# Kernel optimization log

Hardware: AMD Instinct MI355X
Metric: run time of the kernel (lower is better)

The kernel has to match this reference:

```python
import jax, jax.numpy as jnp
import numpy as np
from jax import lax

F_CNT = 64    # factories per player
U_CNT = 2048  # units per player
GRID = 16     # spatial map side after stride-3 conv on 48x48 board


def conv2d(x, w, b, stride=1, pad=1):
    return lax.conv_general_dilated(x, w, (stride, stride), [(pad, pad), (pad, pad)],
                                    dimension_numbers=('NCHW', 'OIHW', 'NCHW')) + b[None, :, None, None]


def prelu(x, a):
    return jnp.where(x > 0, x, a * x)


def linear(x, w, b):
    return x @ w.T + b


def layernorm(x, g, b, eps=1e-5):
    mu = jnp.mean(x, -1, keepdims=True)
    var = jnp.mean((x - mu) ** 2, -1, keepdims=True)
    return (x - mu) / jnp.sqrt(var + eps) * g + b


def maxpool2(x):
    return lax.reduce_window(x, -jnp.inf, lax.max, (1, 1, 2, 2), (1, 1, 2, 2), 'VALID')


def mha4(f0, u0, f1, u1, fw, fb, uw, ub, lw, lb, num_heads=2, hidden=32):
    # FourSequenceMHAttention: per head, per player, separate Q/K/V linears for
    # factories and units; sequence order is [fac_p0, units_p0, fac_p1, units_p1].
    scale = hidden ** 0.5
    heads = []
    for h in range(num_heads):
        Q, K, V = [], [], []
        for i, (f, u) in enumerate(((f0, u0), (f1, u1))):
            b0 = h * 6 + i * 3
            Q.append(linear(f, fw[b0], fb[b0]))
            K.append(linear(f, fw[b0 + 1], fb[b0 + 1]))
            V.append(linear(f, fw[b0 + 2], fb[b0 + 2]))
            Q.append(linear(u, uw[b0], ub[b0]))
            K.append(linear(u, uw[b0 + 1], ub[b0 + 1]))
            V.append(linear(u, uw[b0 + 2], ub[b0 + 2]))
        Qc = jnp.concatenate(Q, 1)
        Kc = jnp.concatenate(K, 1)
        Vc = jnp.concatenate(V, 1)
        attn = jax.nn.softmax(jnp.einsum('bqd,bkd->bqk', Qc, Kc) / scale, axis=-1)
        heads.append(jnp.einsum('bqk,bkd->bqd', attn, Vc))
    return linear(jnp.concatenate(heads, -1), lw, lb)


def scatter_mask(feat, pos, C):
    # one-hot scatter-add of per-unit features onto the 16x16 grid (batch==1)
    gm = jnp.zeros((GRID, GRID, C), feat.dtype).at[pos[:, 0], pos[:, 1]].add(feat[0])
    return jnp.transpose(gm, (2, 0, 1))[None]  # [1,C,16,16]


def _forward(fl, p0_fac_pos, p0_unit_pos, p1_fac_pos, p1_unit_pos):
    (board, p0_fac_feat, p0_unit_feat, p1_fac_feat, p1_unit_feat,
     sp_w1, sp_b1, sp_a1, sp_w2, sp_b2, sp_a2, sp_w3, sp_b3,
     enc_fac_w, enc_fac_b, enc_unit_w, enc_unit_b, enc_lin_w, enc_lin_b,
     ext_fac_w, ext_fac_b, ext_unit_w, ext_unit_b, ext_lin_w, ext_lin_b, ext_ln_g, ext_ln_b,
     v_w1, v_b1, v_a1, v_w2, v_b2, v_a2, v_lw, v_lb,
     fo_w1, fo_b1, fo_a, fo_w2, fo_b2, ro_w1, ro_b1, ro_a, ro_w2, ro_b2) = fl

    sm = prelu(conv2d(board, sp_w1, sp_b1), sp_a1)
    sm = prelu(conv2d(sm, sp_w2, sp_b2), sp_a2)
    sm = conv2d(sm, sp_w3, sp_b3, stride=3, pad=0)  # [1,24,16,16]

    def gather(pos):
        # per-unit gather of the 24-dim spatial feature at (pos_x, pos_y)
        return jnp.transpose(sm[0][:, pos[:, 0], pos[:, 1]], (1, 0))[None]  # [1,N,24]

    f0 = jnp.concatenate([p0_fac_feat, gather(p0_fac_pos)], -1)    # [1,F,31]
    u0 = jnp.concatenate([p0_unit_feat, gather(p0_unit_pos)], -1)  # [1,U,38]
    f1 = jnp.concatenate([p1_fac_feat, gather(p1_fac_pos)], -1)
    u1 = jnp.concatenate([p1_unit_feat, gather(p1_unit_pos)], -1)

    gmu0 = scatter_mask(p0_unit_feat, p0_unit_pos, 14)
    gmf0 = scatter_mask(p0_fac_feat, p0_fac_pos, 7)
    gmu1 = scatter_mask(p1_unit_feat, p1_unit_pos, 14)
    gmf1 = scatter_mask(p1_fac_feat, p1_fac_pos, 7)
    # loop prepends each team's masks: after p1 order is [u1, f1, u0, f0, spatial]
    v_map = jnp.concatenate([gmu1, gmf1, gmu0, gmf0, sm], 1)  # [1,66,16,16]

    seq = mha4(f0, u0, f1, u1, enc_fac_w, enc_fac_b, enc_unit_w, enc_unit_b, enc_lin_w, enc_lin_b)
    S0, S1, S2 = F_CNT, F_CNT + U_CNT, 2 * F_CNT + U_CNT
    for l in range(2):
        new = mha4(seq[:, :S0], seq[:, S0:S1], seq[:, S1:S2], seq[:, S2:],
                   ext_fac_w[l], ext_fac_b[l], ext_unit_w[l], ext_unit_b[l],
                   ext_lin_w[l], ext_lin_b[l])
        seq = layernorm(seq + new, ext_ln_g[l], ext_ln_b[l])

    def head2(x, w1, b1, a, w2, b2):
        return linear(prelu(linear(x, w1, b1), a), w2, b2)

    f0o = head2(seq[:, :S0], fo_w1, fo_b1, fo_a, fo_w2, fo_b2)      # [1,F,4]
    u0o = head2(seq[:, S0:S1], ro_w1, ro_b1, ro_a, ro_w2, ro_b2)    # [1,U,17]
    f1o = head2(seq[:, S1:S2], fo_w1, fo_b1, fo_a, fo_w2, fo_b2)
    u1o = head2(seq[:, S2:], ro_w1, ro_b1, ro_a, ro_w2, ro_b2)

    vm = maxpool2(prelu(conv2d(v_map, v_w1, v_b1), v_a1))  # [1,96,8,8]
    vm = maxpool2(prelu(conv2d(vm, v_w2, v_b2), v_a2))     # [1,128,4,4]
    v = jnp.tanh(vm.reshape(vm.shape[0], -1) @ v_lw.T + v_lb)  # [1,1]
    return (f0o, u0o, f1o, u1o, v)


def setup_inputs() -> dict:
    key = jax.random.key(0)
    ks = iter(jax.random.split(key, 64))

    def rn(shape, s=1.0):
        return s * jax.random.normal(next(ks), shape, dtype=jnp.float32)

    def ri(shape):
        return jax.random.randint(next(ks), shape, 0, GRID)

    a25 = lambda: jnp.full((1,), 0.25, jnp.float32)  # torch PReLU default
    inp = {
        'board': rn((1, 14, 48, 48)),
        'p0_fac_feat': rn((1, F_CNT, 7)), 'p0_unit_feat': rn((1, U_CNT, 14)),
        'p1_fac_feat': rn((1, F_CNT, 7)), 'p1_unit_feat': rn((1, U_CNT, 14)),
        'sp_w1': rn((48, 14, 3, 3), 0.05), 'sp_b1': rn((48,), 0.05), 'sp_a1': a25(),
        'sp_w2': rn((96, 48, 3, 3), 0.05), 'sp_b2': rn((96,), 0.05), 'sp_a2': a25(),
        'sp_w3': rn((24, 96, 3, 3), 0.05), 'sp_b3': rn((24,), 0.05),
        'enc_fac_w': rn((12, 32, 31), 0.05), 'enc_fac_b': rn((12, 32), 0.05),
        'enc_unit_w': rn((12, 32, 38), 0.05), 'enc_unit_b': rn((12, 32), 0.05),
        'enc_lin_w': rn((32, 64), 0.05), 'enc_lin_b': rn((32,), 0.05),
        'ext_fac_w': rn((2, 12, 32, 32), 0.05), 'ext_fac_b': rn((2, 12, 32), 0.05),
        'ext_unit_w': rn((2, 12, 32, 32), 0.05), 'ext_unit_b': rn((2, 12, 32), 0.05),
        'ext_lin_w': rn((2, 32, 64), 0.05), 'ext_lin_b': rn((2, 32), 0.05),
        'ext_ln_g': jnp.ones((2, 32), jnp.float32), 'ext_ln_b': jnp.zeros((2, 32), jnp.float32),
        'v_w1': rn((96, 66, 3, 3), 0.05), 'v_b1': rn((96,), 0.05), 'v_a1': a25(),
        'v_w2': rn((128, 96, 3, 3), 0.05), 'v_b2': rn((128,), 0.05), 'v_a2': a25(),
        'v_lw': rn((1, 128 * 16), 0.05), 'v_lb': rn((1,), 0.05),
        'fo_w1': rn((32, 32), 0.05), 'fo_b1': rn((32,), 0.05), 'fo_a': a25(),
        'fo_w2': rn((4, 32), 0.05), 'fo_b2': rn((4,), 0.05),
        'ro_w1': rn((32, 32), 0.05), 'ro_b1': rn((32,), 0.05), 'ro_a': a25(),
        'ro_w2': rn((17, 32), 0.05), 'ro_b2': rn((17,), 0.05),
        'p0_fac_pos': ri((F_CNT, 2)), 'p0_unit_pos': ri((U_CNT, 2)),
        'p1_fac_pos': ri((F_CNT, 2)), 'p1_unit_pos': ri((U_CNT, 2)),
    }
    return inp


def reference(board, p0_fac_feat, p0_unit_feat, p1_fac_feat, p1_unit_feat,
              sp_w1, sp_b1, sp_a1, sp_w2, sp_b2, sp_a2, sp_w3, sp_b3,
              enc_fac_w, enc_fac_b, enc_unit_w, enc_unit_b, enc_lin_w, enc_lin_b,
              ext_fac_w, ext_fac_b, ext_unit_w, ext_unit_b, ext_lin_w, ext_lin_b, ext_ln_g, ext_ln_b,
              v_w1, v_b1, v_a1, v_w2, v_b2, v_a2, v_lw, v_lb,
              fo_w1, fo_b1, fo_a, fo_w2, fo_b2, ro_w1, ro_b1, ro_a, ro_w2, ro_b2,
              p0_fac_pos, p0_unit_pos, p1_fac_pos, p1_unit_pos):
    fl = (board, p0_fac_feat, p0_unit_feat, p1_fac_feat, p1_unit_feat,
          sp_w1, sp_b1, sp_a1, sp_w2, sp_b2, sp_a2, sp_w3, sp_b3,
          enc_fac_w, enc_fac_b, enc_unit_w, enc_unit_b, enc_lin_w, enc_lin_b,
          ext_fac_w, ext_fac_b, ext_unit_w, ext_unit_b, ext_lin_w, ext_lin_b, ext_ln_g, ext_ln_b,
          v_w1, v_b1, v_a1, v_w2, v_b2, v_a2, v_lw, v_lb,
          fo_w1, fo_b1, fo_a, fo_w2, fo_b2, ro_w1, ro_b1, ro_a, ro_w2, ro_b2)
    return _forward(fl, p0_fac_pos, p0_unit_pos, p1_fac_pos, p1_unit_pos)
```

## Files before the change

### kernel.cpp

```cpp
#include <hip/hip_runtime.h>
#include <hip/hip_bf16.h>

#define SEQ 4224
#define KSPLIT 11
#define KITERS 6
typedef unsigned int uint;
typedef unsigned short ushort;
typedef __attribute__((ext_vector_type(8))) short bf16x8;
typedef __attribute__((ext_vector_type(4))) float f32x4;

__device__ __forceinline__ float prelu_f(float x, float a){ return x > 0.f ? x : a*x; }

__device__ __forceinline__ ushort bfr(float x){
  uint u = __float_as_uint(x);
  u = (u + 0x7fffu + ((u>>16)&1u)) >> 16;
  return (ushort)u;
}
__device__ __forceinline__ uint pkbf(float a, float b){
  __hip_bfloat162 h2 = __float22bfloat162_rn(make_float2(a,b));
  union { __hip_bfloat162 h; uint u; } cv; cv.h = h2; return cv.u;
}

#define QSCALE 0.25505607190037247f
#define FIXEDM 8.0f

struct MegaParams {
  const float *board,*p0f,*p0u,*p1f,*p1u;
  const float *sp_w1,*sp_b1,*sp_a1,*sp_w2,*sp_b2,*sp_a2,*sp_w3,*sp_b3;
  const float *enc_fac_w,*enc_fac_b,*enc_unit_w,*enc_unit_b,*enc_lin_w,*enc_lin_b;
  const float *ext_fac_w,*ext_fac_b,*ext_unit_w,*ext_unit_b,*ext_lin_w,*ext_lin_b,*ext_ln_g,*ext_ln_b;
  const float *v_w1,*v_b1,*v_a1,*v_w2,*v_b2,*v_a2,*v_lw,*v_lb;
  const float *fo_w1,*fo_b1,*fo_a,*fo_w2,*fo_b2,*ro_w1,*ro_b1,*ro_a,*ro_w2,*ro_b2;
  const int *p0fp,*p0up,*p1fp,*p1up;
  float* out;
  float *sm1,*sm2,*sm;
  ushort *q16,*k16,*vt16;
  float *Hp,*auxl,*seqA,*seqB,*vmap,*vp1,*vp2;
};

template<int CIN, int HW, int CPT>
__device__ __forceinline__ void conv_item(int cg_, int pxb, int tid,
    const float* __restrict__ in, const float* __restrict__ w,
    const float* __restrict__ bias, const float* __restrict__ alpha,
    float* __restrict__ out, float* SF){
  float* Ws = SF;
  float* Bs = SF + CPT*CIN*9;
  for (int idx=tid; idx<CPT*CIN*9; idx+=256) Ws[idx] = w[cg_*CPT*CIN*9 + idx];
  if (tid<CPT) Bs[tid] = bias[cg_*CPT+tid];
  __syncthreads();
  int p = pxb*256 + tid;
  int x = p % HW, y = p / HW;
  float a = alpha[0];
  float acc[CPT];
  #pragma unroll
  for (int c=0;c<CPT;++c) acc[c]=Bs[c];
  #pragma unroll 2
  for (int i=0;i<CIN;++i){
    const float* ip = in + i*HW*HW;
    float win[9];
    #pragma unroll
    for (int ky=0;ky<3;++ky){
      int yy = y+ky-1;
      #pragma unroll
      for (int kx=0;kx<3;++kx){
        int xx = x+kx-1;
        bool ok = ((unsigned)yy < (unsigned)HW) && ((unsigned)xx < (unsigned)HW);
        win[ky*3+kx] = ok ? ip[yy*HW+xx] : 0.f;
      }
    }
    #pragma unroll
    for (int c=0;c<CPT;++c){
      const float* wp = &Ws[(c*CIN+i)*9];
      #pragma unroll
      for (int k=0;k<9;++k) acc[c] += win[k]*wp[k];
    }
  }
  #pragma unroll
  for (int c=0;c<CPT;++c)
    out[(cg_*CPT+c)*HW*HW + p] = prelu_f(acc[c], a);
}

__device__ __forceinline__ void scatter_item(int e, const MegaParams& P){
  if (e>=SEQ) return;
  const float* feat; const int* pos; int n, ch0, C;
  if (e<2048){ n=e; feat=P.p1u+n*14; pos=P.p1up; ch0=0; C=14; }
  else if (e<2112){ n=e-2048; feat=P.p1f+n*7; pos=P.p1fp; ch0=14; C=7; }
  else if (e<4160){ n=e-2112; feat=P.p0u+n*14; pos=P.p0up; ch0=21; C=14; }
  else { n=e-4160; feat=P.p0f+n*7; pos=P.p0fp; ch0=35; C=7; }
  int off = pos[2*n]*16 + pos[2*n+1];
  for (int c=0;c<C;++c) atomicAdd(&P.vmap[(ch0+c)*256 + off], feat[c]);
}

__device__ __forceinline__ void qkv_item(int blk, int tid, const MegaParams* GP,
    const float* x0, const float* x1, const float* x2, const float* x3,
    int ind_f, int ind_u,
    const float* fw, const float* fb, const float* uw, const float* ub,
    ushort* Q16, ushort* K16, ushort* VT16, float* SF){
  float* Xs = SF;
  float* Ws = SF + 2560;
  float* Bs = SF + 3840;
  int chunk = blk % 66;
  int hm = blk / 66;
  int m = hm >> 1, h = hm & 1;
  const float* xb=nullptr; int ind, isfac, pl;
  if (chunk==0){ xb=x0; ind=ind_f; isfac=1; pl=0; }
  else if (chunk<=32){ xb = x1 ? x1 + (size_t)(chunk-1)*64*ind_u : nullptr; ind=ind_u; isfac=0; pl=0; }
  else if (chunk==33){ xb=x2; ind=ind_f; isfac=1; pl=1; }
  else { xb = x3 ? x3 + (size_t)(chunk-34)*64*ind_u : nullptr; ind=ind_u; isfac=0; pl=1; }
  int b0 = h*6 + pl*3 + m;
  const float* w = (isfac? fw:uw) + (size_t)b0*32*ind;
  const float* bias = (isfac? fb:ub) + b0*32;
  {
    int r = tid>>2, seg = tid&3;
    if (GP){
      const float* feat; const int* pos; int nf, n;
      if (chunk==0){ n=r; feat=GP->p0f+n*7; pos=GP->p0fp; nf=7; }
      else if (chunk<=32){ n=(chunk-1)*64+r; feat=GP->p0u+(size_t)n*14; pos=GP->p0up; nf=14; }
      else if (chunk==33){ n=r; feat=GP->p1f+n*7; pos=GP->p1fp; nf=7; }
      else { n=(chunk-34)*64+r; feat=GP->p1u+(size_t)n*14; pos=GP->p1up; nf=14; }
      int px = pos[2*n], py = pos[2*n+1];
      const float* s = GP->sm + px*16 + py;
      #pragma unroll
      for (int j=0;j<10;++j){
        int c = seg*10+j;
        float v;
        if (c<nf) v = feat[c];
        else if (c<ind) v = s[(c-nf)*256];
        else v = 0.f;
        Xs[r*40+c] = v;
      }
    } else {
      const float* xr = xb + (size_t)r*ind;
      #pragma unroll
      for (int j=0;j<10;++j){ int c = seg*10+j; Xs[r*40+c] = (c<ind) ? xr[c] : 0.f; }
    }
    int o = tid>>3, sg = tid&7;
    const float* wr = w + (size_t)o*ind;
    #pragma unroll
    for (int j=0;j<5;++j){ int c = sg*5+j; Ws[o*40+c] = (c<ind) ? wr[c] : 0.f; }
    if (tid<32) Bs[tid]=bias[tid];
  }
  __syncthreads();
  int og = tid&7, rg = tid>>3;
  const float4* Xs4 = (const float4*)Xs;
  const float4* Ws4 = (const float4*)Ws;
  float acc[2][4];
  #pragma unroll
  for (int k=0;k<4;++k){ float b = Bs[og+8*k]; acc[0][k]=b; acc[1][k]=b; }
  #pragma unroll
  for (int d4=0; d4<10; ++d4){
    float4 xa = Xs4[rg*10+d4];
    float4 xb2 = Xs4[(rg+32)*10+d4];
    #pragma unroll
    for (int k=0;k<4;++k){
      float4 wv = Ws4[(og+8*k)*10+d4];
      acc[0][k] += xa.x*wv.x + xa.y*wv.y + xa.z*wv.z + xa.w*wv.w;
      acc[1][k] += xb2.x*wv.x + xb2.y*wv.y + xb2.z*wv.z + xb2.w*wv.w;
    }
  }
  if (m==0){
    #pragma unroll
    for (int j=0;j<2;++j){
      int r = rg + 32*j;
      ushort* base = Q16 + ((size_t)h*SEQ + chunk*64 + r)*32;
      #pragma unroll
      for (int k=0;k<4;++k) base[og+8*k] = bfr(acc[j][k]*QSCALE);
    }
  } else if (m==1){
    #pragma unroll
    for (int j=0;j<2;++j){
      int r = rg + 32*j;
      ushort* base = K16 + ((size_t)h*SEQ + chunk*64 + r)*32;
      #pragma unroll
      for (int k=0;k<4;++k) base[og+8*k] = bfr(acc[j][k]);
    }
  } else {
    #pragma unroll
    for (int k=0;k<4;++k){
      ushort* base = VT16 + ((size_t)h*32 + og+8*k)*SEQ + chunk*64;
      #pragma unroll
      for (int j=0;j<2;++j) base[rg+32*j] = bfr(acc[j][k]);
    }
  }
}

__device__ __forceinline__ void flash_item(int item, int tid,
    const ushort* Q16, const ushort* K16, const ushort* VT16,
    float* Hpart, float* auxl, ushort* SU){
  ushort* KsB = SU;
  ushort* VTB = SU + 5120;
  ushort* PlB = SU + 10240;
  int qb = item % 66, h = (item/66)&1, ks = item/132;
  int wv = tid>>6, l = tid&63, lq = l&15, g = l>>4;
  const ushort* Qh = Q16 + (size_t)h*SEQ*32;
  const ushort* Kh = K16 + (size_t)h*SEQ*32;
  const ushort* VTh = VT16 + (size_t)h*32*SEQ;

  bf16x8 qf = *(const bf16x8*)(Qh + (size_t)(qb*64 + wv*16 + lq)*32 + g*8);

  int krow = tid>>2, kc8 = (tid&3)*8;
  int vd = tid>>3, vk8 = (tid&7)*8;

  f32x4 o0 = {0.f,0.f,0.f,0.f}, o1 = {0.f,0.f,0.f,0.f};
  float lrow = 0.f;

  int kt0 = ks*KITERS;
  bf16x8 kpre = *(const bf16x8*)(Kh + (size_t)(kt0*64 + krow)*32 + kc8);
  bf16x8 vpre = *(const bf16x8*)(VTh + (size_t)vd*SEQ + kt0*64 + vk8);
  *(bf16x8*)&KsB[0*2560 + krow*40 + kc8] = kpre;
  *(bf16x8*)&VTB[0*2560 + vd*80 + vk8] = vpre;

  for (int it=0; it<KITERS; ++it){
    int pb = it&1;
    if (it+1 < KITERS){
      kpre = *(const bf16x8*)(Kh + (size_t)((kt0+it+1)*64 + krow)*32 + kc8);
      vpre = *(const bf16x8*)(VTh + (size_t)vd*SEQ + (kt0+it+1)*64 + vk8);
    }
    __syncthreads();
    f32x4 z = {0.f,0.f,0.f,0.f};
    f32x4 sT[4];
    #pragma unroll
    for (int m=0;m<4;++m){
      bf16x8 kf = *(const bf16x8*)&KsB[pb*2560 + (16*m+lq)*40 + g*8];
      sT[m] = __builtin_amdgcn_mfma_f32_16x16x32_bf16(kf, qf, z, 0, 0, 0);
    }
    float ts = 0.f;
    #pragma unroll
    for (int m=0;m<4;++m){
      #pragma unroll
      for (int r=0;r<4;++r){ float p = exp2f(sT[m][r]-FIXEDM); sT[m][r]=p; ts+=p; }
    }
    ts += __shfl_xor(ts,16); ts += __shfl_xor(ts,32);
    lrow += ts;
    #pragma unroll
    for (int m=0;m<4;++m){
      uint2 pw; pw.x = pkbf(sT[m][0],sT[m][1]); pw.y = pkbf(sT[m][2],sT[m][3]);
      *(uint2*)&PlB[wv*1152 + lq*72 + 16*m + g*4] = pw;
    }
    #pragma unroll
    for (int s=0;s<2;++s){
      bf16x8 pf = *(const bf16x8*)&PlB[wv*1152 + lq*72 + s*32 + g*8];
      bf16x8 vf0 = *(const bf16x8*)&VTB[pb*2560 + lq*80 + s*32 + g*8];
      bf16x8 vf1 = *(const bf16x8*)&VTB[pb*2560 + (lq+16)*80 + s*32 + g*8];
      o0 = __builtin_amdgcn_mfma_f32_16x16x32_bf16(pf, vf0, o0, 0, 0, 0);
      o1 = __builtin_amdgcn_mfma_f32_16x16x32_bf16(pf, vf1, o1, 0, 0, 0);
    }
    if (it+1 < KITERS){
      *(bf16x8*)&KsB[(pb^1)*2560 + krow*40 + kc8] = kpre;
      *(bf16x8*)&VTB[(pb^1)*2560 + vd*80 + vk8] = vpre;
    }
  }
  int qg0 = qb*64 + wv*16;
  #pragma unroll
  for (int r=0;r<4;++r){
    size_t row = (size_t)ks*SEQ + qg0 + g*4 + r;
    Hpart[row*64 + h*32 + lq]      = o0[r];
    Hpart[row*64 + h*32 + lq + 16] = o1[r];
  }
  if (g==0) auxl[(size_t)(ks*2+h)*SEQ + qg0 + lq] = lrow;
}

__device__ __forceinline__ float combine_row(const float* Hp, const float* auxl, int s, int d){
  int hh = d>>5;
  float den = 0.f, hv = 0.f;
  #pragma unroll
  for (int p=0;p<KSPLIT;++p){
    den += auxl[(size_t)(p*2+hh)*SEQ + s];
    hv  += Hp[(size_t)p*SEQ*64 + (size_t)s*64 + d];
  }
  return hv/den;
}

__device__ __forceinline__ void outlin_item(int blk, int tid,
    const float* Hp, const float* auxl, const float* lw, const float* lb,
    const float* seqin, const float* g, const float* b, float* seqout,
    bool LN, float* SF){
  float* Ls = SF;
  float* Hc = SF + 2176;
  int s0 = blk*8;
  for (int idx=tid; idx<2048; idx+=256){ int o=idx>>6, d=idx&63; Ls[o*68+d]=lw[idx]; }
  for (int idx=tid; idx<512; idx+=256){
    int sl = idx>>6, d = idx&63;
    Hc[sl*68+d] = combine_row(Hp, auxl, s0+sl, d);
  }
  __syncthreads();
  int o = tid&31, sl = tid>>5;
  const float4* H4 = (const float4*)&Hc[sl*68];
  const float4* L4 = (const float4*)&Ls[o*68];
  float acc = lb[o] + (LN ? seqin[(s0+sl)*32+o] : 0.f);
  #pragma unroll
  for (int d4=0; d4<16; ++d4){
    float4 hv = H4[d4], lv = L4[d4];
    acc += hv.x*lv.x + hv.y*lv.y + hv.z*lv.z + hv.w*lv.w;
  }
  if (LN){
    float sum=acc;
    #pragma unroll
    for (int off=1; off<32; off<<=1) sum += __shfl_xor(sum,off);
    float mu = sum*0.03125f;
    float dv = acc-mu;
    float vs = dv*dv;
    #pragma unroll
    for (int off=1; off<32; off<<=1) vs += __shfl_xor(vs,off);
    float rstd = rsqrtf(vs*0.03125f + 1e-5f);
    seqout[(s0+sl)*32+o] = dv*rstd*g[o] + b[o];
  } else {
    seqout[(s0+sl)*32+o] = acc;
  }
}

__device__ __forceinline__ void qkv_layer(const MegaParams& P, int layer, int blk, int tid, float* SF){
  if (layer==0)
    qkv_item(blk, tid, &P, nullptr,nullptr,nullptr,nullptr, 31,38,
        P.enc_fac_w,P.enc_fac_b,P.enc_unit_w,P.enc_unit_b, P.q16,P.k16,P.vt16, SF);
  else if (layer==1)
    qkv_item(blk, tid, nullptr, P.seqA, P.seqA+64*32, P.seqA+2112*32, P.seqA+2176*32, 32,32,
        P.ext_fac_w,P.ext_fac_b,P.ext_unit_w,P.ext_unit_b, P.q16,P.k16,P.vt16, SF);
  else
    qkv_item(blk, tid, nullptr, P.seqB, P.seqB+64*32, P.seqB+2112*32, P.seqB+2176*32, 32,32,
        P.ext_fac_w+12288,P.ext_fac_b+384,P.ext_unit_w+12288,P.ext_unit_b+384, P.q16,P.k16,P.vt16, SF);
}
__device__ __forceinline__ void outlin_layer(const MegaParams& P, int layer, int blk, int tid, float* SF){
  if (layer==0)
    outlin_item(blk,tid,P.Hp,P.auxl,P.enc_lin_w,P.enc_lin_b,nullptr,nullptr,nullptr,P.seqA,false,SF);
  else if (layer==1)
    outlin_item(blk,tid,P.Hp,P.auxl,P.ext_lin_w,P.ext_lin_b,P.seqA,P.ext_ln_g,P.ext_ln_b,P.seqB,true,SF);
  else
    outlin_item(blk,tid,P.Hp,P.auxl,P.ext_lin_w+2048,P.ext_lin_b+32,P.seqB,P.ext_ln_g+32,P.ext_ln_b+32,P.seqA,true,SF);
}

__device__ __forceinline__ void vconv1_item(int item2, int tid, const MegaParams& P, float* SF){
  float* In = SF;
  float* Wc = SF + 6336;
  int c = item2>>2, q = item2&3;
  int y0 = q*4;
  const float4* vm4 = (const float4*)P.vmap;
  const float4* sm4 = (const float4*)P.sm;
  float4* In4 = (float4*)In;
  for (int idx4=tid; idx4<1584; idx4+=256){
    int i = idx4/24, rem = idx4 - i*24;
    int r = rem>>2, x4 = rem&3;
    int y = y0 - 1 + r;
    float4 v;
    if ((unsigned)y < 16u) v = (i<42) ? vm4[i*64 + y*4 + x4] : sm4[(i-42)*64 + y*4 + x4];
    else { v.x=v.y=v.z=v.w=0.f; }
    In4[idx4] = v;
  }
  for (int idx=tid; idx<594; idx+=256) Wc[idx] = P.v_w1[c*594 + idx];
  __syncthreads();
  if (tid<64){
    int x = tid & 15, ry = tid >> 4;
    float a = P.v_a1[0];
    float acc = P.v_b1[c];
    for (int i=0;i<66;++i){
      const float* base = &In[i*96 + ry*16];
      const float* wp = &Wc[i*9];
      #pragma unroll
      for (int ky=0;ky<3;++ky){
        const float* row = base + ky*16;
        #pragma unroll
        for (int kx=0;kx<3;++kx){
          int xx = x+kx-1;
          float v = ((unsigned)xx<16u) ? row[xx] : 0.f;
          acc += v*wp[ky*3+kx];
        }
      }
    }
    acc = prelu_f(acc, a);
    float mx = fmaxf(acc, __shfl_xor(acc,1));
    mx = fmaxf(mx, __shfl_xor(mx,16));
    if (((x&1)==0) && ((ry&1)==0))
      P.vp1[c*64 + (q*2 + (ry>>1))*8 + (x>>1)] = mx;
  }
}

__device__ __forceinline__ void vconv2_item(int c, int tid, const MegaParams& P, float* SF){
  float* In = SF;
  float* Ws = SF + 6144;
  const float4* in4 = (const float4*)P.vp1;
  float4* In4 = (float4*)In;
  for (int idx4=tid; idx4<1536; idx4+=256) In4[idx4] = in4[idx4];
  for (int idx=tid; idx<864; idx+=256) Ws[idx] = P.v_w2[c*864 + idx];
  __syncthreads();
  if (tid<64){
    int x = tid&7, y = tid>>3;
    float acc = P.v_b2[c];
    for (int i=0;i<96;++i){
      const float* base = &In[i*64];
      const float* wp = &Ws[i*9];
      #pragma unroll
      for (int ky=0;ky<3;++ky){
        int yy = y+ky-1;
        #pragma unroll
        for (int kx=0;kx<3;++kx){
          int xx = x+kx-1;
          bool ok = ((unsigned)yy<8u) && ((unsigned)xx<8u);
          float v = ok ? base[yy*8+xx] : 0.f;
          acc += v*wp[ky*3+kx];
        }
      }
    }
    acc = prelu_f(acc, P.v_a2[0]);
    float mx = fmaxf(acc, __shfl_xor(acc,1));
    mx = fmaxf(mx, __shfl_xor(mx,8));
    if (((x&1)==0) && ((y&1)==0))
      P.vp2[c*16 + (y>>1)*4 + (x>>1)] = mx;
  }
}

__device__ __forceinline__ void vfinal_item(int tid, const MegaParams& P, float* SF){
  float* red = SF;
  float s=0.f;
  for (int i=tid;i<2048;i+=256) s += P.vp2[i]*P.v_lw[i];
  red[tid]=s; __syncthreads();
  for (int k=128;k>0;k>>=1){ if (tid<k) red[tid]+=red[tid+k]; __syncthreads(); }
  if (tid==0) P.out[70144] = tanhf(red[0]+P.v_lb[0]);
}

__global__ __launch_bounds__(256) void k_conv1z(MegaParams P){
  __shared__ __align__(16) float SF[512];
  if (blockIdx.x < 108)
    conv_item<14,48,4>(blockIdx.x/9, blockIdx.x%9, threadIdx.x, P.board,P.sp_w1,P.sp_b1,P.sp_a1,P.sm1,SF);
  else
    P.vmap[(blockIdx.x-108)*256+threadIdx.x] = 0.f;
}
__global__ __launch_bounds__(256) void k_conv2x(MegaParams P){
  __shared__ __align__(16) float SF[872];
  int b = blockIdx.x;
  if (b < 432)
    conv_item<48,48,2>(b/9, b%9, threadIdx.x, P.sm1,P.sp_w2,P.sp_b2,P.sp_a2,P.sm2,SF);
  else if (b < 449)
    scatter_item((b-432)*256+threadIdx.x, P);
  else {
    int base = (b-449)*1024;
    #pragma unroll
    for (int j=0;j<4;++j) P.sm[base + j*256 + threadIdx.x] = 0.f;
  }
}
__global__ __launch_bounds__(256) void k_convs3(MegaParams P){
  __shared__ __align__(16) float Ws[432];
  int c = blockIdx.x>>1, half = blockIdx.x&1;
  int tid = threadIdx.x;
  for (int idx=tid; idx<432; idx+=256) Ws[idx] = P.sp_w3[c*864 + half*432 + idx];
  __syncthreads();
  int x = tid&15, y = tid>>4;
  float acc = half ? 0.f : P.sp_b3[c];
  const float* ip0 = P.sm2 + (size_t)half*48*2304 + y*144 + x*3;
  #pragma unroll 4
  for (int i=0;i<48;++i){
    const float* ip = ip0 + i*2304;
    float win[9];
    #pragma unroll
    for (int ky=0;ky<3;++ky)
      #pragma unroll
      for (int kx=0;kx<3;++kx) win[ky*3+kx] = ip[ky*48+kx];
    const float* w0 = &Ws[i*9];
    #pragma unroll
    for (int k=0;k<9;++k) acc += win[k]*w0[k];
  }
  atomicAdd(&P.sm[c*256 + y*16 + x], acc);
}
__global__ __launch_bounds__(256) void k_qkv0_vc1(MegaParams P){
  __shared__ __align__(16) float SF[6930];
  if (blockIdx.x < 396) qkv_layer(P, 0, blockIdx.x, threadIdx.x, SF);
  else vconv1_item(blockIdx.x-396, threadIdx.x, P, SF);
}
__global__ __launch_bounds__(256) void k_flash(MegaParams P){
  __shared__ __align__(16) char SM[29696];
  flash_item(blockIdx.x, threadIdx.x, P.q16,P.k16,P.vt16,P.Hp,P.auxl,(ushort*)SM);
}
__global__ __launch_bounds__(256) void k_outlin0_vc2(MegaParams P){
  __shared__ __align__(16) float SF[7008];
  if (blockIdx.x < 528) outlin_layer(P, 0, blockIdx.x, threadIdx.x, SF);
  else vconv2_item(blockIdx.x-528, threadIdx.x, P, SF);
}
__global__ __launch_bounds__(256) void k_qkv1_vf(MegaParams P){
  __shared__ __align__(16) float SF[3904];
  if (blockIdx.x < 396) qkv_layer(P, 1, blockIdx.x, threadIdx.x, SF);
  else vfinal_item(threadIdx.x, P, SF);
}
__global__ __launch_bounds__(256) void k_qkv(MegaParams P, int layer){
  __shared__ __align__(16) float SF[3904];
  qkv_layer(P, layer, blockIdx.x, threadIdx.x, SF);
}
__global__ __launch_bounds__(256) void k_outlin(MegaParams P, int layer){
  __shared__ __align__(16) float SF[2720];
  outlin_layer(P, layer, blockIdx.x, threadIdx.x, SF);
}
__global__ __launch_bounds__(256) void k_head2(MegaParams P){
  __shared__ float W1f[1024], W1r[1024], W2f[128], W2r[544];
  __shared__ float B1f[32], B1r[32], B2f[4], B2r[17];
  int tid = threadIdx.x;
  for (int i=tid;i<1024;i+=256){ W1f[i]=P.fo_w1[i]; W1r[i]=P.ro_w1[i]; }
  for (int i=tid;i<544;i+=256) W2r[i]=P.ro_w2[i];
  if (tid<128) W2f[tid]=P.fo_w2[tid];
  if (tid<32){ B1f[tid]=P.fo_b1[tid]; B1r[tid]=P.ro_b1[tid]; }
  if (tid<17) B2r[tid]=P.ro_b2[tid];
  if (tid<4)  B2f[tid]=P.fo_b2[tid];
  __syncthreads();
  int e = blockIdx.x*256+tid;
  if (e>=SEQ) return;
  const float *w1,*b1,*w2,*b2; float a; int od; float* dst;
  float* out = P.out;
  if (e<64){ w1=W1f;b1=B1f;a=P.fo_a[0];w2=W2f;b2=B2f;od=4; dst=out + e*4; }
  else if (e<2112){ w1=W1r;b1=B1r;a=P.ro_a[0];w2=W2r;b2=B2r;od=17; dst=out + 256 + (size_t)(e-64)*17; }
  else if (e<2176){ w1=W1f;b1=B1f;a=P.fo_a[0];w2=W2f;b2=B2f;od=4; dst=out + 35072 + (e-2112)*4; }
  else { w1=W1r;b1=B1r;a=P.ro_a[0];w2=W2r;b2=B2r;od=17; dst=out + 35328 + (size_t)(e-2176)*17; }
  float x[32];
  #pragma unroll
  for (int i=0;i<32;++i) x[i]=P.seqA[(size_t)e*32+i];
  float hbuf[32];
  #pragma unroll
  for (int j=0;j<32;++j){
    float acc=b1[j];
    #pragma unroll
    for (int i=0;i<32;++i) acc+=w1[j*32+i]*x[i];
    hbuf[j]=prelu_f(acc,a);
  }
  for (int k=0;k<od;++k){
    float acc=b2[k];
    #pragma unroll
    for (int j=0;j<32;++j) acc+=w2[k*32+j]*hbuf[j];
    dst[k]=acc;
  }
}

extern "C" void kernel_launch(void* const* d_in, const int* in_sizes, int n_in,
                              void* d_out, int out_size, void* d_ws, size_t ws_size,
                              hipStream_t stream){
  (void)in_sizes; (void)n_in; (void)out_size; (void)ws_size;
  MegaParams P;
  P.board=(const float*)d_in[0];
  P.p0f=(const float*)d_in[1]; P.p0u=(const float*)d_in[2];
  P.p1f=(const float*)d_in[3]; P.p1u=(const float*)d_in[4];
  P.sp_w1=(const float*)d_in[5]; P.sp_b1=(const float*)d_in[6]; P.sp_a1=(const float*)d_in[7];
  P.sp_w2=(const float*)d_in[8]; P.sp_b2=(const float*)d_in[9]; P.sp_a2=(const float*)d_in[10];
  P.sp_w3=(const float*)d_in[11]; P.sp_b3=(const float*)d_in[12];
  P.enc_fac_w=(const float*)d_in[13]; P.enc_fac_b=(const float*)d_in[14];
  P.enc_unit_w=(const float*)d_in[15]; P.enc_unit_b=(const float*)d_in[16];
  P.enc_lin_w=(const float*)d_in[17]; P.enc_lin_b=(const float*)d_in[18];
  P.ext_fac_w=(const float*)d_in[19]; P.ext_fac_b=(const float*)d_in[20];
  P.ext_unit_w=(const float*)d_in[21]; P.ext_unit_b=(const float*)d_in[22];
  P.ext_lin_w=(const float*)d_in[23]; P.ext_lin_b=(const float*)d_in[24];
  P.ext_ln_g=(const float*)d_in[25]; P.ext_ln_b=(const float*)d_in[26];
  P.v_w1=(const float*)d_in[27]; P.v_b1=(const float*)d_in[28]; P.v_a1=(const float*)d_in[29];
  P.v_w2=(const float*)d_in[30]; P.v_b2=(const float*)d_in[31]; P.v_a2=(const float*)d_in[32];
  P.v_lw=(const float*)d_in[33]; P.v_lb=(const float*)d_in[34];
  P.fo_w1=(const float*)d_in[35]; P.fo_b1=(const float*)d_in[36]; P.fo_a=(const float*)d_in[37];
  P.fo_w2=(const float*)d_in[38]; P.fo_b2=(const float*)d_in[39];
  P.ro_w1=(const float*)d_in[40]; P.ro_b1=(const float*)d_in[41]; P.ro_a=(const float*)d_in[42];
  P.ro_w2=(const float*)d_in[43]; P.ro_b2=(const float*)d_in[44];
  P.p0fp=(const int*)d_in[45]; P.p0up=(const int*)d_in[46];
  P.p1fp=(const int*)d_in[47]; P.p1up=(const int*)d_in[48];
  P.out = (float*)d_out;

  float* W = (float*)d_ws;
  P.sm1 = W;
  P.sm2 = P.sm1 + 110592;
  P.sm  = P.sm2 + 221184;
  P.q16 = (ushort*)(P.sm + 6144);
  P.k16 = P.q16 + 2*SEQ*32;
  P.vt16 = P.k16 + 2*SEQ*32;
  P.Hp  = (float*)(P.vt16 + 2*SEQ*32);
  P.auxl = P.Hp + KSPLIT*SEQ*64;
  P.seqA = P.auxl + KSPLIT*2*SEQ;
  P.seqB = P.seqA + SEQ*32;
  P.vmap = P.seqB + SEQ*32;
  P.vp1  = P.vmap + 66*256;
  P.vp2  = P.vp1 + 96*64;

  k_conv1z<<<150,256,0,stream>>>(P);
  k_conv2x<<<455,256,0,stream>>>(P);
  k_convs3<<<48,256,0,stream>>>(P);
  k_qkv0_vc1<<<780,256,0,stream>>>(P);
  k_flash<<<1452,256,0,stream>>>(P);
  k_outlin0_vc2<<<656,256,0,stream>>>(P);
  k_qkv1_vf<<<397,256,0,stream>>>(P);
  k_flash<<<1452,256,0,stream>>>(P);
  k_outlin<<<528,256,0,stream>>>(P,1);
  k_qkv<<<396,256,0,stream>>>(P,2);
  k_flash<<<1452,256,0,stream>>>(P);
  k_outlin<<<528,256,0,stream>>>(P,2);
  k_head2<<<17,256,0,stream>>>(P);
}
```

Before: 336.5 us.

## Fuse output-linear into next QKV projection and into the final heads

The per-layer output-projection kernels are removed. Each QKV block now recombines the split-K attention partials and applies the output linear (plus residual and layernorm) for its own 64-row chunk directly into shared memory. The last output linear is merged with the two MLP heads, and the second value-conv stage moves into the first flash-attention launch, cutting launches from 13 to 10 and avoiding intermediate round trips. In exchange, the partial-sum combine and output linear are recomputed by all six head/matrix blocks per chunk, which multiplies reads of the large partial buffer and serialises eight sync-separated sub-steps per block.

```diff
diff --git a/kernel.cpp b/kernel.cpp
--- a/kernel.cpp
+++ b/kernel.cpp
@@ -91,56 +91,9 @@
   for (int c=0;c<C;++c) atomicAdd(&P.vmap[(ch0+c)*256 + off], feat[c]);
 }
 
-__device__ __forceinline__ void qkv_item(int blk, int tid, const MegaParams* GP,
-    const float* x0, const float* x1, const float* x2, const float* x3,
-    int ind_f, int ind_u,
-    const float* fw, const float* fb, const float* uw, const float* ub,
-    ushort* Q16, ushort* K16, ushort* VT16, float* SF){
-  float* Xs = SF;
-  float* Ws = SF + 2560;
-  float* Bs = SF + 3840;
-  int chunk = blk % 66;
-  int hm = blk / 66;
-  int m = hm >> 1, h = hm & 1;
-  const float* xb=nullptr; int ind, isfac, pl;
-  if (chunk==0){ xb=x0; ind=ind_f; isfac=1; pl=0; }
-  else if (chunk<=32){ xb = x1 ? x1 + (size_t)(chunk-1)*64*ind_u : nullptr; ind=ind_u; isfac=0; pl=0; }
-  else if (chunk==33){ xb=x2; ind=ind_f; isfac=1; pl=1; }
-  else { xb = x3 ? x3 + (size_t)(chunk-34)*64*ind_u : nullptr; ind=ind_u; isfac=0; pl=1; }
-  int b0 = h*6 + pl*3 + m;
-  const float* w = (isfac? fw:uw) + (size_t)b0*32*ind;
-  const float* bias = (isfac? fb:ub) + b0*32;
-  {
-    int r = tid>>2, seg = tid&3;
-    if (GP){
-      const float* feat; const int* pos; int nf, n;
-      if (chunk==0){ n=r; feat=GP->p0f+n*7; pos=GP->p0fp; nf=7; }
-      else if (chunk<=32){ n=(chunk-1)*64+r; feat=GP->p0u+(size_t)n*14; pos=GP->p0up; nf=14; }
-      else if (chunk==33){ n=r; feat=GP->p1f+n*7; pos=GP->p1fp; nf=7; }
-      else { n=(chunk-34)*64+r; feat=GP->p1u+(size_t)n*14; pos=GP->p1up; nf=14; }
-      int px = pos[2*n], py = pos[2*n+1];
-      const float* s = GP->sm + px*16 + py;
-      #pragma unroll
-      for (int j=0;j<10;++j){
-        int c = seg*10+j;
-        float v;
-        if (c<nf) v = feat[c];
-        else if (c<ind) v = s[(c-nf)*256];
-        else v = 0.f;
-        Xs[r*40+c] = v;
-      }
-    } else {
-      const float* xr = xb + (size_t)r*ind;
-      #pragma unroll
-      for (int j=0;j<10;++j){ int c = seg*10+j; Xs[r*40+c] = (c<ind) ? xr[c] : 0.f; }
-    }
-    int o = tid>>3, sg = tid&7;
-    const float* wr = w + (size_t)o*ind;
-    #pragma unroll
-    for (int j=0;j<5;++j){ int c = sg*5+j; Ws[o*40+c] = (c<ind) ? wr[c] : 0.f; }
-    if (tid<32) Bs[tid]=bias[tid];
-  }
-  __syncthreads();
+__device__ __forceinline__ void qkv_mm_tail(int chunk, int m, int h, int tid,
+    const float* Xs, const float* Ws, const float* Bs,
+    ushort* Q16, ushort* K16, ushort* VT16){
   int og = tid&7, rg = tid>>3;
   const float4* Xs4 = (const float4*)Xs;
   const float4* Ws4 = (const float4*)Ws;
@@ -182,6 +135,137 @@
       for (int j=0;j<2;++j) base[rg+32*j] = bfr(acc[j][k]);
     }
   }
+}
+
+__device__ __forceinline__ void qkv0_item(int blk, int tid, const MegaParams& P, float* SF){
+  float* Xs = SF;
+  float* Ws = SF + 2560;
+  float* Bs = SF + 3840;
+  int chunk = blk % 66;
+  int hm = blk / 66;
+  int m = hm >> 1, h = hm & 1;
+  int ind, isfac, pl;
+  if (chunk==0){ ind=31; isfac=1; pl=0; }
+  else if (chunk<=32){ ind=38; isfac=0; pl=0; }
+  else if (chunk==33){ ind=31; isfac=1; pl=1; }
+  else { ind=38; isfac=0; pl=1; }
+  int b0 = h*6 + pl*3 + m;
+  const float* w = (isfac? P.enc_fac_w:P.enc_unit_w) + (size_t)b0*32*ind;
+  const float* bias = (isfac? P.enc_fac_b:P.enc_unit_b) + b0*32;
+  {
+    int r = tid>>2, seg = tid&3;
+    const float* feat; const int* pos; int nf, n;
+    if (chunk==0){ n=r; feat=P.p0f+n*7; pos=P.p0fp; nf=7; }
+    else if (chunk<=32){ n=(chunk-1)*64+r; feat=P.p0u+(size_t)n*14; pos=P.p0up; nf=14; }
+    else if (chunk==33){ n=r; feat=P.p1f+n*7; pos=P.p1fp; nf=7; }
+    else { n=(chunk-34)*64+r; feat=P.p1u+(size_t)n*14; pos=P.p1up; nf=14; }
+    int px = pos[2*n], py = pos[2*n+1];
+    const float* s = P.sm + px*16 + py;
+    #pragma unroll
+    for (int j=0;j<10;++j){
+      int c = seg*10+j;
+      float v;
+      if (c<nf) v = feat[c];
+      else if (c<ind) v = s[(c-nf)*256];
+      else v = 0.f;
+      Xs[r*40+c] = v;
+    }
+    int o = tid>>3, sg = tid&7;
+    const float* wr = w + (size_t)o*ind;
+    #pragma unroll
+    for (int j=0;j<5;++j){ int c = sg*5+j; Ws[o*40+c] = (c<ind) ? wr[c] : 0.f; }
+    if (tid<32) Bs[tid]=bias[tid];
+  }
+  __syncthreads();
+  qkv_mm_tail(chunk, m, h, tid, Xs, Ws, Bs, P.q16, P.k16, P.vt16);
+}
+
+__device__ __forceinline__ float combine_row(const float* Hp, const float* auxl, int s, int d){
+  int hh = d>>5;
+  float den = 0.f, hv = 0.f;
+  #pragma unroll
+  for (int p=0;p<KSPLIT;++p){
+    den += auxl[(size_t)(p*2+hh)*SEQ + s];
+    hv  += Hp[(size_t)p*SEQ*64 + (size_t)s*64 + d];
+  }
+  return hv/den;
+}
+
+__device__ __forceinline__ void outlin_to_Xs(int chunk, int tid,
+    const float* Hp, const float* auxl, const float* lw, const float* lb,
+    const float* seqin, const float* g, const float* b, bool LN,
+    float* seqwr, float* Xs, float* Ls, float* Hc){
+  for (int idx=tid; idx<2048; idx+=256){ int o=idx>>6, d=idx&63; Ls[o*68+d]=lw[idx]; }
+  for (int idx=tid; idx<512; idx+=256){ int r=idx>>3, c=32+(idx&7); Xs[r*40+c]=0.f; }
+  int o = tid&31, sl = tid>>5;
+  for (int rr=0; rr<8; ++rr){
+    int srow0 = chunk*64 + rr*8;
+    __syncthreads();
+    for (int idx=tid; idx<512; idx+=256){
+      int s2=idx>>6, d=idx&63;
+      Hc[s2*68+d] = combine_row(Hp, auxl, srow0+s2, d);
+    }
+    __syncthreads();
+    int s = srow0 + sl;
+    const float4* H4 = (const float4*)&Hc[sl*68];
+    const float4* L4 = (const float4*)&Ls[o*68];
+    float acc = lb[o] + (LN ? seqin[(size_t)s*32+o] : 0.f);
+    #pragma unroll
+    for (int d4=0; d4<16; ++d4){
+      float4 hv = H4[d4], lv = L4[d4];
+      acc += hv.x*lv.x + hv.y*lv.y + hv.z*lv.z + hv.w*lv.w;
+    }
+    if (LN){
+      float sum=acc;
+      #pragma unroll
+      for (int off=1; off<32; off<<=1) sum += __shfl_xor(sum,off);
+      float mu = sum*0.03125f;
+      float dv = acc-mu;
+      float vs = dv*dv;
+      #pragma unroll
+      for (int off=1; off<32; off<<=1) vs += __shfl_xor(vs,off);
+      float rstd = rsqrtf(vs*0.03125f + 1e-5f);
+      acc = dv*rstd*g[o] + b[o];
+    }
+    Xs[(rr*8+sl)*40 + o] = acc;
+    if (seqwr) seqwr[(size_t)s*32+o] = acc;
+  }
+}
+
+__device__ __forceinline__ void qkvf_item(int blk, int tid, const MegaParams& P, int layer, float* SF){
+  float* Xs = SF;
+  float* Ws = SF + 2560;
+  float* Bs = SF + 3840;
+  float* Ls = SF + 3872;
+  float* Hc = SF + 6048;
+  int chunk = blk % 66;
+  int hm = blk / 66;
+  int m = hm >> 1, h = hm & 1;
+  if (layer==1){
+    outlin_to_Xs(chunk, tid, P.Hp, P.auxl, P.enc_lin_w, P.enc_lin_b,
+        nullptr, nullptr, nullptr, false, (hm==0)? P.seqA : nullptr, Xs, Ls, Hc);
+  } else {
+    outlin_to_Xs(chunk, tid, P.Hp, P.auxl, P.ext_lin_w, P.ext_lin_b,
+        P.seqA, P.ext_ln_g, P.ext_ln_b, true, (hm==0)? P.seqB : nullptr, Xs, Ls, Hc);
+  }
+  int isfac = (chunk==0 || chunk==33);
+  int pl = (chunk<33) ? 0 : 1;
+  int b0 = h*6 + pl*3 + m;
+  const float* fw = (layer==1) ? P.ext_fac_w  : P.ext_fac_w+12288;
+  const float* fb = (layer==1) ? P.ext_fac_b  : P.ext_fac_b+384;
+  const float* uw = (layer==1) ? P.ext_unit_w : P.ext_unit_w+12288;
+  const float* ub = (layer==1) ? P.ext_unit_b : P.ext_unit_b+384;
+  const float* w = (isfac? fw:uw) + (size_t)b0*32*32;
+  const float* bias = (isfac? fb:ub) + b0*32;
+  {
+    int o = tid>>3, sg = tid&7;
+    const float* wr = w + (size_t)o*32;
+    #pragma unroll
+    for (int j=0;j<5;++j){ int c = sg*5+j; Ws[o*40+c] = (c<32) ? wr[c] : 0.f; }
+    if (tid<32) Bs[tid]=bias[tid];
+  }
+  __syncthreads();
+  qkv_mm_tail(chunk, m, h, tid, Xs, Ws, Bs, P.q16, P.k16, P.vt16);
 }
 
 __device__ __forceinline__ void flash_item(int item, int tid,
@@ -258,75 +342,6 @@
     Hpart[row*64 + h*32 + lq + 16] = o1[r];
   }
   if (g==0) auxl[(size_t)(ks*2+h)*SEQ + qg0 + lq] = lrow;
-}
-
-__device__ __forceinline__ float combine_row(const float* Hp, const float* auxl, int s, int d){
-  int hh = d>>5;
-  float den = 0.f, hv = 0.f;
-  #pragma unroll
-  for (int p=0;p<KSPLIT;++p){
-    den += auxl[(size_t)(p*2+hh)*SEQ + s];
-    hv  += Hp[(size_t)p*SEQ*64 + (size_t)s*64 + d];
-  }
-  return hv/den;
-}
-
-__device__ __forceinline__ void outlin_item(int blk, int tid,
-    const float* Hp, const float* auxl, const float* lw, const float* lb,
-    const float* seqin, const float* g, const float* b, float* seqout,
-    bool LN, float* SF){
-  float* Ls = SF;
-  float* Hc = SF + 2176;
-  int s0 = blk*8;
-  for (int idx=tid; idx<2048; idx+=256){ int o=idx>>6, d=idx&63; Ls[o*68+d]=lw[idx]; }
-  for (int idx=tid; idx<512; idx+=256){
-    int sl = idx>>6, d = idx&63;
-    Hc[sl*68+d] = combine_row(Hp, auxl, s0+sl, d);
-  }
-  __syncthreads();
-  int o = tid&31, sl = tid>>5;
-  const float4* H4 = (const float4*)&Hc[sl*68];
-  const float4* L4 = (const float4*)&Ls[o*68];
-  float acc = lb[o] + (LN ? seqin[(s0+sl)*32+o] : 0.f);
-  #pragma unroll
-  for (int d4=0; d4<16; ++d4){
-    float4 hv = H4[d4], lv = L4[d4];
-    acc += hv.x*lv.x + hv.y*lv.y + hv.z*lv.z + hv.w*lv.w;
-  }
-  if (LN){
-    float sum=acc;
-    #pragma unroll
-    for (int off=1; off<32; off<<=1) sum += __shfl_xor(sum,off);
-    float mu = sum*0.03125f;
-    float dv = acc-mu;
-    float vs = dv*dv;
-    #pragma unroll
-    for (int off=1; off<32; off<<=1) vs += __shfl_xor(vs,off);
-    float rstd = rsqrtf(vs*0.03125f + 1e-5f);
-    seqout[(s0+sl)*32+o] = dv*rstd*g[o] + b[o];
-  } else {
-    seqout[(s0+sl)*32+o] = acc;
-  }
-}
-
-__device__ __forceinline__ void qkv_layer(const MegaParams& P, int layer, int blk, int tid, float* SF){
-  if (layer==0)
-    qkv_item(blk, tid, &P, nullptr,nullptr,nullptr,nullptr, 31,38,
-        P.enc_fac_w,P.enc_fac_b,P.enc_unit_w,P.enc_unit_b, P.q16,P.k16,P.vt16, SF);
-  else if (layer==1)
-    qkv_item(blk, tid, nullptr, P.seqA, P.seqA+64*32, P.seqA+2112*32, P.seqA+2176*32, 32,32,
-        P.ext_fac_w,P.ext_fac_b,P.ext_unit_w,P.ext_unit_b, P.q16,P.k16,P.vt16, SF);
-  else
-    qkv_item(blk, tid, nullptr, P.seqB, P.seqB+64*32, P.seqB+2112*32, P.seqB+2176*32, 32,32,
-        P.ext_fac_w+12288,P.ext_fac_b+384,P.ext_unit_w+12288,P.ext_unit_b+384, P.q16,P.k16,P.vt16, SF);
-}
-__device__ __forceinline__ void outlin_layer(const MegaParams& P, int layer, int blk, int tid, float* SF){
-  if (layer==0)
-    outlin_item(blk,tid,P.Hp,P.auxl,P.enc_lin_w,P.enc_lin_b,nullptr,nullptr,nullptr,P.seqA,false,SF);
-  else if (layer==1)
-    outlin_item(blk,tid,P.Hp,P.auxl,P.ext_lin_w,P.ext_lin_b,P.seqA,P.ext_ln_g,P.ext_ln_b,P.seqB,true,SF);
-  else
-    outlin_item(blk,tid,P.Hp,P.auxl,P.ext_lin_w+2048,P.ext_lin_b+32,P.seqB,P.ext_ln_g+32,P.ext_ln_b+32,P.seqA,true,SF);
 }
 
 __device__ __forceinline__ void vconv1_item(int item2, int tid, const MegaParams& P, float* SF){
@@ -462,66 +477,100 @@
 }
 __global__ __launch_bounds__(256) void k_qkv0_vc1(MegaParams P){
   __shared__ __align__(16) float SF[6930];
-  if (blockIdx.x < 396) qkv_layer(P, 0, blockIdx.x, threadIdx.x, SF);
+  if (blockIdx.x < 396) qkv0_item(blockIdx.x, threadIdx.x, P, SF);
   else vconv1_item(blockIdx.x-396, threadIdx.x, P, SF);
+}
+__global__ __launch_bounds__(256) void k_flash0_vc2(MegaParams P){
+  __shared__ __align__(16) char SM[29696];
+  if (blockIdx.x < 1452) flash_item(blockIdx.x, threadIdx.x, P.q16,P.k16,P.vt16,P.Hp,P.auxl,(ushort*)SM);
+  else vconv2_item(blockIdx.x-1452, threadIdx.x, P, (float*)SM);
 }
 __global__ __launch_bounds__(256) void k_flash(MegaParams P){
   __shared__ __align__(16) char SM[29696];
   flash_item(blockIdx.x, threadIdx.x, P.q16,P.k16,P.vt16,P.Hp,P.auxl,(ushort*)SM);
 }
-__global__ __launch_bounds__(256) void k_outlin0_vc2(MegaParams P){
-  __shared__ __align__(16) float SF[7008];
-  if (blockIdx.x < 528) outlin_layer(P, 0, blockIdx.x, threadIdx.x, SF);
-  else vconv2_item(blockIdx.x-528, threadIdx.x, P, SF);
-}
-__global__ __launch_bounds__(256) void k_qkv1_vf(MegaParams P){
-  __shared__ __align__(16) float SF[3904];
-  if (blockIdx.x < 396) qkv_layer(P, 1, blockIdx.x, threadIdx.x, SF);
+__global__ __launch_bounds__(256) void k_qkvf1_vf(MegaParams P){
+  __shared__ __align__(16) float SF[6592];
+  if (blockIdx.x < 396) qkvf_item(blockIdx.x, threadIdx.x, P, 1, SF);
   else vfinal_item(threadIdx.x, P, SF);
 }
-__global__ __launch_bounds__(256) void k_qkv(MegaParams P, int layer){
-  __shared__ __align__(16) float SF[3904];
-  qkv_layer(P, layer, blockIdx.x, threadIdx.x, SF);
-}
-__global__ __launch_bounds__(256) void k_outlin(MegaParams P, int layer){
-  __shared__ __align__(16) float SF[2720];
-  outlin_layer(P, layer, blockIdx.x, threadIdx.x, SF);
-}
-__global__ __launch_bounds__(256) void k_head2(MegaParams P){
+__global__ __launch_bounds__(256) void k_qkvf2(MegaParams P){
+  __shared__ __align__(16) float SF[6592];
+  qkvf_item(blockIdx.x, threadIdx.x, P, 2, SF);
+}
+__global__ __launch_bounds__(256) void k_outlin_head(MegaParams P){
+  __shared__ __align__(16) float Ls[2176];
+  __shared__ __align__(16) float Hc[544];
+  __shared__ float Xr[8*33], Hb[8*33];
   __shared__ float W1f[1024], W1r[1024], W2f[128], W2r[544];
   __shared__ float B1f[32], B1r[32], B2f[4], B2r[17];
   int tid = threadIdx.x;
+  const float* lw = P.ext_lin_w + 2048;
+  const float* lb = P.ext_lin_b + 32;
+  const float* g  = P.ext_ln_g + 32;
+  const float* bb = P.ext_ln_b + 32;
+  for (int idx=tid; idx<2048; idx+=256){ int o=idx>>6, d=idx&63; Ls[o*68+d]=lw[idx]; }
   for (int i=tid;i<1024;i+=256){ W1f[i]=P.fo_w1[i]; W1r[i]=P.ro_w1[i]; }
   for (int i=tid;i<544;i+=256) W2r[i]=P.ro_w2[i];
   if (tid<128) W2f[tid]=P.fo_w2[tid];
   if (tid<32){ B1f[tid]=P.fo_b1[tid]; B1r[tid]=P.ro_b1[tid]; }
   if (tid<17) B2r[tid]=P.ro_b2[tid];
   if (tid<4)  B2f[tid]=P.fo_b2[tid];
-  __syncthreads();
-  int e = blockIdx.x*256+tid;
-  if (e>=SEQ) return;
-  const float *w1,*b1,*w2,*b2; float a; int od; float* dst;
-  float* out = P.out;
-  if (e<64){ w1=W1f;b1=B1f;a=P.fo_a[0];w2=W2f;b2=B2f;od=4; dst=out + e*4; }
-  else if (e<2112){ w1=W1r;b1=B1r;a=P.ro_a[0];w2=W2r;b2=B2r;od=17; dst=out + 256 + (size_t)(e-64)*17; }
-  else if (e<2176){ w1=W1f;b1=B1f;a=P.fo_a[0];w2=W2f;b2=B2f;od=4; dst=out + 35072 + (e-2112)*4; }
-  else { w1=W1r;b1=B1r;a=P.ro_a[0];w2=W2r;b2=B2r;od=17; dst=out + 35328 + (size_t)(e-2176)*17; }
-  float x[32];
-  #pragma unroll
-  for (int i=0;i<32;++i) x[i]=P.seqA[(size_t)e*32+i];
-  float hbuf[32];
-  #pragma unroll
-  for (int j=0;j<32;++j){
-    float acc=b1[j];
-    #pragma unroll
-    for (int i=0;i<32;++i) acc+=w1[j*32+i]*x[i];
-    hbuf[j]=prelu_f(acc,a);
-  }
-  for (int k=0;k<od;++k){
-    float acc=b2[k];
-    #pragma unroll
-    for (int j=0;j<32;++j) acc+=w2[k*32+j]*hbuf[j];
-    dst[k]=acc;
+  int s0 = blockIdx.x*8;
+  for (int idx=tid; idx<512; idx+=256){
+    int s2=idx>>6, d=idx&63;
+    Hc[s2*68+d] = combine_row(P.Hp, P.auxl, s0+s2, d);
+  }
+  __syncthreads();
+  int o = tid&31, sl = tid>>5;
+  int s = s0 + sl;
+  {
+    const float4* H4 = (const float4*)&Hc[sl*68];
+    const float4* L4 = (const float4*)&Ls[o*68];
+    float acc = lb[o] + P.seqB[(size_t)s*32+o];
+    #pragma unroll
+    for (int d4=0; d4<16; ++d4){
+      float4 hv = H4[d4], lv = L4[d4];
+      acc += hv.x*lv.x + hv.y*lv.y + hv.z*lv.z + hv.w*lv.w;
+    }
+    float sum=acc;
+    #pragma unroll
+    for (int off=1; off<32; off<<=1) sum += __shfl_xor(sum,off);
+    float mu = sum*0.03125f;
+    float dv = acc-mu;
+    float vs = dv*dv;
+    #pragma unroll
+    for (int off=1; off<32; off<<=1) vs += __shfl_xor(vs,off);
+    float rstd = rsqrtf(vs*0.03125f + 1e-5f);
+    Xr[sl*33+o] = dv*rstd*g[o] + bb[o];
+  }
+  __syncthreads();
+  bool isfac = (s<64) || (s>=2112 && s<2176);
+  float a = isfac ? P.fo_a[0] : P.ro_a[0];
+  const float* w1 = isfac ? W1f : W1r;
+  const float* b1 = isfac ? B1f : B1r;
+  {
+    float acc = b1[o];
+    const float* xr = &Xr[sl*33];
+    #pragma unroll
+    for (int i=0;i<32;++i) acc += w1[o*32+i]*xr[i];
+    Hb[sl*33+o] = prelu_f(acc, a);
+  }
+  __syncthreads();
+  int od = isfac ? 4 : 17;
+  if (o < od){
+    const float* w2 = isfac ? W2f : W2r;
+    const float* b2 = isfac ? B2f : B2r;
+    float acc = b2[o];
+    const float* hb = &Hb[sl*33];
+    #pragma unroll
+    for (int j=0;j<32;++j) acc += w2[o*32+j]*hb[j];
+    float* dst;
+    if (s<64) dst = P.out + s*4;
+    else if (s<2112) dst = P.out + 256 + (size_t)(s-64)*17;
+    else if (s<2176) dst = P.out + 35072 + (s-2112)*4;
+    else dst = P.out + 35328 + (size_t)(s-2176)*17;
+    dst[o] = acc;
   }
 }
 
@@ -573,13 +622,10 @@
   k_conv2x<<<455,256,0,stream>>>(P);
   k_convs3<<<48,256,0,stream>>>(P);
   k_qkv0_vc1<<<780,256,0,stream>>>(P);
+  k_flash0_vc2<<<1580,256,0,stream>>>(P);
+  k_qkvf1_vf<<<397,256,0,stream>>>(P);
   k_flash<<<1452,256,0,stream>>>(P);
-  k_outlin0_vc2<<<656,256,0,stream>>>(P);
-  k_qkv1_vf<<<397,256,0,stream>>>(P);
+  k_qkvf2<<<396,256,0,stream>>>(P);
   k_flash<<<1452,256,0,stream>>>(P);
-  k_outlin<<<528,256,0,stream>>>(P,1);
-  k_qkv<<<396,256,0,stream>>>(P,2);
-  k_flash<<<1452,256,0,stream>>>(P);
-  k_outlin<<<528,256,0,stream>>>(P,2);
-  k_head2<<<17,256,0,stream>>>(P);
-}
+  k_outlin_head<<<528,256,0,stream>>>(P);
+}
```

Result: slower. 372.8 us (+10.8%).
